# Performance work log

Hardware: AMD Instinct MI355X
Metric: run time of the kernel (lower is better)

The kernel has to match this reference:

```python
import jax, jax.numpy as jnp
import numpy as np

B, T, D_IN, D_EMB, H = 4, 2048, 1024, 1024, 16
HD = D_EMB // H  # head_dim = 64


def setup_inputs() -> dict:
    key = jax.random.key(0)
    k1, k2, k3 = jax.random.split(key, 3)
    scale_qkv = 1.0 / np.sqrt(D_IN)
    scale_o = 1.0 / np.sqrt(D_EMB)
    return {
        "x": jax.random.normal(k1, (B, T, D_IN), dtype=jnp.float32),
        "w_qkv": jax.random.normal(k2, (3 * D_EMB, D_IN), dtype=jnp.float32) * scale_qkv,
        "w_o": jax.random.normal(k3, (D_EMB, D_EMB), dtype=jnp.float32) * scale_o,
        "b_o": jnp.zeros((D_EMB,), dtype=jnp.float32),
    }


def reference(x, w_qkv, w_o, b_o):
    Bv, Tv, _ = x.shape
    # qkv projection: [B,T,3*D_EMB] -> [B,H,T,3*HD]
    qkv = jnp.einsum('btd,ed->bte', x, w_qkv)
    qkv = qkv.reshape(Bv, Tv, H, 3 * HD).transpose(0, 2, 1, 3)
    q, k, v = jnp.split(qkv, 3, axis=-1)  # each [B,H,T,HD]
    # scaled dot product with causal mask
    logits = jnp.einsum('bhqd,bhkd->bhqk', q, k) / np.sqrt(HD)
    causal = jnp.tril(jnp.ones((Tv, Tv), dtype=bool))
    logits = jnp.where(causal, logits, -jnp.inf)
    attn = jax.nn.softmax(logits, axis=-1)
    vals = jnp.einsum('bhqk,bhkd->bhqd', attn, v)
    vals = vals.transpose(0, 2, 1, 3).reshape(Bv, Tv, D_EMB)
    return jnp.einsum('bte,oe->bto', vals, w_o) + b_o
```

## Files before the change

### kernel.cpp

```cpp
#include <hip/hip_runtime.h>
#include <hip/hip_bf16.h>
#include <cstdint>
#include <cstddef>

#define B_    4
#define T_    2048
#define DIN_  1024
#define DEMB_ 1024
#define H_    16
#define HD_   64
#define M_    8192
#define NQKV_ 3072

#define QSCALE 0.18033688011112042f

typedef __bf16 bf16_t;
typedef __bf16 bf16x8 __attribute__((ext_vector_type(8)));
typedef __bf16 bf16x4 __attribute__((ext_vector_type(4)));
typedef float  f32x4  __attribute__((ext_vector_type(4)));
typedef float  f32x16 __attribute__((ext_vector_type(16)));
typedef unsigned int u32x4 __attribute__((ext_vector_type(4)));

__device__ __forceinline__ bf16_t tob(float f) {
  __hip_bfloat16 h = __float2bfloat16(f);
  return __builtin_bit_cast(bf16_t, h);
}

__device__ __forceinline__ f32x4 mfma16(bf16x8 a, bf16x8 b, f32x4 c) {
  return __builtin_amdgcn_mfma_f32_16x16x32_bf16(a, b, c, 0, 0, 0);
}
__device__ __forceinline__ f32x16 mfma32(bf16x8 a, bf16x8 b, f32x16 c) {
  return __builtin_amdgcn_mfma_f32_32x32x16_bf16(a, b, c, 0, 0, 0);
}

__device__ __forceinline__ float fexp2(float x) {
#if __has_builtin(__builtin_amdgcn_exp2f)
  return __builtin_amdgcn_exp2f(x);
#else
  return exp2f(x);
#endif
}

__device__ __forceinline__ unsigned pk2(float lo, float hi) {
  unsigned r;
  asm("v_cvt_pk_bf16_f32 %0, %1, %2" : "=v"(r) : "v"(lo), "v"(hi));
  return r;
}

__device__ __forceinline__ void plswap(unsigned& a, unsigned& b) {
  asm("v_permlane32_swap_b32 %0, %1" : "+v"(a), "+v"(b));
}

__device__ __forceinline__ void gload16(const void* g, void* l) {
  __builtin_amdgcn_global_load_lds((const __attribute__((address_space(1))) void*)g,
                                   (__attribute__((address_space(3))) void*)l, 16, 0, 0);
}

__global__ __launch_bounds__(256) void cast3_kernel(const float* __restrict__ a, bf16_t* __restrict__ ao,
                                                    const float* __restrict__ b, bf16_t* __restrict__ bo,
                                                    const float* __restrict__ c, bf16_t* __restrict__ co) {
  constexpr int na4 = M_ * DIN_ / 4;
  constexpr int nb4 = NQKV_ * DIN_ / 4;
  const int i = blockIdx.x * 256 + threadIdx.x;
  const float* src; bf16_t* dst; int off;
  if (i < na4)            { src = a; dst = ao; off = i; }
  else if (i < na4 + nb4) { src = b; dst = bo; off = i - na4; }
  else                    { src = c; dst = co; off = i - na4 - nb4; }
  float4 v = ((const float4*)src)[off];
  bf16x4 o;
  o[0] = tob(v.x); o[1] = tob(v.y); o[2] = tob(v.z); o[3] = tob(v.w);
  ((bf16x4*)dst)[off] = o;
}

__global__ __launch_bounds__(256, 3) void gemm_qkv_kernel(const bf16_t* __restrict__ A,
                                                          const bf16_t* __restrict__ Bm,
                                                          bf16_t* __restrict__ qb,
                                                          bf16_t* __restrict__ kb,
                                                          bf16_t* __restrict__ vbT) {
  constexpr int K = DIN_;
  __shared__ __align__(16) bf16_t As[128 * 64];
  __shared__ __align__(16) bf16_t Bs[128 * 64];
  const int tid = threadIdx.x, w = tid >> 6, l = tid & 63;
  const int lh = l >> 4, lr = l & 15;
  const int m0 = blockIdx.y * 128, n0 = blockIdx.x * 128;
  const int ar0 = (w >> 1) * 64, bc0 = (w & 1) * 64;
  f32x4 acc[4][4] = {};
  for (int k0 = 0; k0 < K; k0 += 64) {
#pragma unroll
    for (int i = 0; i < 4; ++i) {
      const int jx = i * 256 + tid;
      const int row = jx >> 3, us = (jx & 7) ^ (row & 7);
      gload16(A  + (size_t)(m0 + row) * K + k0 + us * 8, (char*)As + (size_t)(i * 256 + w * 64) * 16);
      gload16(Bm + (size_t)(n0 + row) * K + k0 + us * 8, (char*)Bs + (size_t)(i * 256 + w * 64) * 16);
    }
    __syncthreads();
#pragma unroll
    for (int kk = 0; kk < 2; ++kk) {
      bf16x8 af[4], bfv[4];
#pragma unroll
      for (int mi = 0; mi < 4; ++mi) {
        const int r = ar0 + mi * 16 + lr;
        af[mi] = *(const bf16x8*)&As[r * 64 + (((kk * 4 + lh) ^ (r & 7)) * 8)];
      }
#pragma unroll
      for (int ni = 0; ni < 4; ++ni) {
        const int r = bc0 + ni * 16 + lr;
        bfv[ni] = *(const bf16x8*)&Bs[r * 64 + (((kk * 4 + lh) ^ (r & 7)) * 8)];
      }
      __builtin_amdgcn_s_setprio(1);
#pragma unroll
      for (int mi = 0; mi < 4; ++mi)
#pragma unroll
        for (int ni = 0; ni < 4; ++ni)
          acc[mi][ni] = mfma16(af[mi], bfv[ni], acc[mi][ni]);
      __builtin_amdgcn_s_setprio(0);
    }
    __syncthreads();
  }
#pragma unroll
  for (int mi = 0; mi < 4; ++mi) {
    const int gm0 = m0 + ar0 + mi * 16 + lh * 4;
    const int bb = gm0 >> 11, t0 = gm0 & (T_ - 1);
#pragma unroll
    for (int ni = 0; ni < 4; ++ni) {
      const int gn = n0 + bc0 + ni * 16 + lr;
      const int h = gn / 192, s = gn - h * 192;
      const size_t bhb = (size_t)bb * H_ + h;
      if (s < 64) {
#pragma unroll
        for (int r = 0; r < 4; ++r)
          qb[(bhb * T_ + t0 + r) * HD_ + s] = tob(acc[mi][ni][r] * QSCALE);
      } else if (s < 128) {
#pragma unroll
        for (int r = 0; r < 4; ++r)
          kb[(bhb * T_ + t0 + r) * HD_ + s - 64] = tob(acc[mi][ni][r]);
      } else {
        bf16x4 pv;
#pragma unroll
        for (int r = 0; r < 4; ++r) pv[r] = tob(acc[mi][ni][r]);
        *(bf16x4*)&vbT[(bhb * HD_ + (s - 128)) * T_ + t0] = pv;
      }
    }
  }
}

__global__ __launch_bounds__(256, 2) void attn2_kernel(const bf16_t* __restrict__ qg,
                                                       const bf16_t* __restrict__ kg,
                                                       const bf16_t* __restrict__ vtg,
                                                       bf16_t* __restrict__ ob) {
  __shared__ __align__(16) bf16_t Kl[2][64 * 72];
  __shared__ __align__(16) bf16_t Vl[2][64 * 72];
  const int id = blockIdx.x;
  const int x  = (id >> 3) & 7;
  const int bh = (id & 7) | ((id >> 6) << 3);
  const int tid = threadIdx.x, w = tid >> 6, l = tid & 63;
  const int q5 = l & 31, hi = l >> 5, hi8 = hi * 8;
  const int srow = tid >> 3, scol = (tid & 7) * 8;
  const bf16_t* Qg  = qg  + (size_t)bh * T_ * HD_;
  const bf16_t* Kg  = kg  + (size_t)bh * T_ * HD_;
  const bf16_t* Vtg = vtg + (size_t)bh * HD_ * T_;

  for (int ph = 0; ph < 2; ++ph) {
    const int qt = ph ? (15 - x) : x;
    const int qb = qt * 128 + w * 32;
    const int ktmax = 2 * qt + 2;
    const int myKt  = qb >> 6;
    const int thrD  = qb + q5 - myKt * 64 - 4 * hi;

    bf16x8 bq[4];
#pragma unroll
    for (int s = 0; s < 4; ++s)
      bq[s] = *(const bf16x8*)&Qg[(size_t)(qb + q5) * HD_ + s * 16 + hi8];

    f32x16 o0 = {}, o1 = {};
    float lrun = 0.f;

    {
      *(bf16x8*)&Kl[0][srow * 72 + scol]        = *(const bf16x8*)&Kg[(size_t)srow * HD_ + scol];
      *(bf16x8*)&Kl[0][(srow + 32) * 72 + scol] = *(const bf16x8*)&Kg[(size_t)(srow + 32) * HD_ + scol];
      *(bf16x8*)&Vl[0][srow * 72 + scol]        = *(const bf16x8*)&Vtg[(size_t)srow * T_ + scol];
      *(bf16x8*)&Vl[0][(srow + 32) * 72 + scol] = *(const bf16x8*)&Vtg[(size_t)(srow + 32) * T_ + scol];
    }
    __syncthreads();
    int cur = 0;

    for (int kt = 0; kt < ktmax; ++kt) {
      const bool more = (kt + 1 < ktmax);
      bf16x8 nk0, nk1, nv0, nv1;
      if (more) {
        nk0 = *(const bf16x8*)&Kg[(size_t)((kt + 1) * 64 + srow) * HD_ + scol];
        nk1 = *(const bf16x8*)&Kg[(size_t)((kt + 1) * 64 + srow + 32) * HD_ + scol];
        nv0 = *(const bf16x8*)&Vtg[(size_t)srow * T_ + (kt + 1) * 64 + scol];
        nv1 = *(const bf16x8*)&Vtg[(size_t)(srow + 32) * T_ + (kt + 1) * 64 + scol];
      }
      if (kt <= myKt) {
        f32x16 sA = {}, sB = {};
        __builtin_amdgcn_s_setprio(1);
#pragma unroll
        for (int s = 0; s < 4; ++s) {
          bf16x8 a0 = *(const bf16x8*)&Kl[cur][(q5)      * 72 + s * 16 + hi8];
          bf16x8 a1 = *(const bf16x8*)&Kl[cur][(q5 + 32) * 72 + s * 16 + hi8];
          sA = mfma32(a0, bq[s], sA);
          sB = mfma32(a1, bq[s], sB);
        }
        __builtin_amdgcn_s_setprio(0);
        if (kt == myKt) {
#pragma unroll
          for (int r = 0; r < 16; ++r) {
            const int kvc = (r & 3) + 8 * (r >> 2);
            sA[r] = (kvc      > thrD) ? -1e30f : sA[r];
            sB[r] = (kvc + 32 > thrD) ? -1e30f : sB[r];
          }
        }
        float l0 = 0.f, l1 = 0.f, l2 = 0.f, l3 = 0.f;
#pragma unroll
        for (int r = 0; r < 16; r += 4) {
          sA[r]     = fexp2(sA[r]);     sB[r]     = fexp2(sB[r]);
          sA[r + 1] = fexp2(sA[r + 1]); sB[r + 1] = fexp2(sB[r + 1]);
          sA[r + 2] = fexp2(sA[r + 2]); sB[r + 2] = fexp2(sB[r + 2]);
          sA[r + 3] = fexp2(sA[r + 3]); sB[r + 3] = fexp2(sB[r + 3]);
          l0 += sA[r]     + sB[r];
          l1 += sA[r + 1] + sB[r + 1];
          l2 += sA[r + 2] + sB[r + 2];
          l3 += sA[r + 3] + sB[r + 3];
        }
        lrun += (l0 + l1) + (l2 + l3);
#pragma unroll
        for (int t32 = 0; t32 < 2; ++t32) {
          const f32x16& p = t32 ? sB : sA;
#pragma unroll
          for (int s2 = 0; s2 < 2; ++s2) {
            unsigned a0 = pk2(p[8 * s2 + 0], p[8 * s2 + 1]);
            unsigned a1 = pk2(p[8 * s2 + 2], p[8 * s2 + 3]);
            unsigned b0 = pk2(p[8 * s2 + 4], p[8 * s2 + 5]);
            unsigned b1 = pk2(p[8 * s2 + 6], p[8 * s2 + 7]);
            plswap(a0, b0);
            plswap(a1, b1);
            u32x4 fw = {a0, a1, b0, b1};
            const bf16x8 pb = __builtin_bit_cast(bf16x8, fw);
            const int kvo = t32 * 32 + s2 * 16 + hi8;
            bf16x8 av0 = *(const bf16x8*)&Vl[cur][(q5)      * 72 + kvo];
            bf16x8 av1 = *(const bf16x8*)&Vl[cur][(q5 + 32) * 72 + kvo];
            __builtin_amdgcn_s_setprio(1);
            o0 = mfma32(av0, pb, o0);
            o1 = mfma32(av1, pb, o1);
            __builtin_amdgcn_s_setprio(0);
          }
        }
      }
      if (more) {
        *(bf16x8*)&Kl[cur ^ 1][srow * 72 + scol]        = nk0;
        *(bf16x8*)&Kl[cur ^ 1][(srow + 32) * 72 + scol] = nk1;
        *(bf16x8*)&Vl[cur ^ 1][srow * 72 + scol]        = nv0;
        *(bf16x8*)&Vl[cur ^ 1][(srow + 32) * 72 + scol] = nv1;
      }
      __syncthreads();
      cur ^= 1;
    }

    const float ltot = lrun + __shfl_xor(lrun, 32);
    const float inv = 1.f / ltot;
    const size_t rowb = ((size_t)(bh >> 4) * T_ + qb + q5) * DEMB_ + (bh & 15) * HD_;
#pragma unroll
    for (int g = 0; g < 4; ++g) {
      bf16x4 st0, st1;
#pragma unroll
      for (int j = 0; j < 4; ++j) {
        st0[j] = tob(o0[4 * g + j] * inv);
        st1[j] = tob(o1[4 * g + j] * inv);
      }
      *(bf16x4*)&ob[rowb + 8 * g + 4 * hi]      = st0;
      *(bf16x4*)&ob[rowb + 8 * g + 4 * hi + 32] = st1;
    }
  }
}

__global__ __launch_bounds__(256, 3) void gemm_out_kernel(const bf16_t* __restrict__ A,
                                                          const bf16_t* __restrict__ Bm,
                                                          const float* __restrict__ bo,
                                                          float* __restrict__ out) {
  constexpr int K = DEMB_;
  __shared__ __align__(16) bf16_t As[128 * 64];
  __shared__ __align__(16) bf16_t Bs[128 * 64];
  const int tid = threadIdx.x, w = tid >> 6, l = tid & 63;
  const int lh = l >> 4, lr = l & 15;
  const int m0 = blockIdx.y * 128, n0 = blockIdx.x * 128;
  const int ar0 = (w >> 1) * 64, bc0 = (w & 1) * 64;
  f32x4 acc[4][4] = {};
  for (int k0 = 0; k0 < K; k0 += 64) {
#pragma unroll
    for (int i = 0; i < 4; ++i) {
      const int jx = i * 256 + tid;
      const int row = jx >> 3, us = (jx & 7) ^ (row & 7);
      gload16(A  + (size_t)(m0 + row) * K + k0 + us * 8, (char*)As + (size_t)(i * 256 + w * 64) * 16);
      gload16(Bm + (size_t)(n0 + row) * K + k0 + us * 8, (char*)Bs + (size_t)(i * 256 + w * 64) * 16);
    }
    __syncthreads();
#pragma unroll
    for (int kk = 0; kk < 2; ++kk) {
      bf16x8 af[4], bfv[4];
#pragma unroll
      for (int mi = 0; mi < 4; ++mi) {
        const int r = ar0 + mi * 16 + lr;
        af[mi] = *(const bf16x8*)&As[r * 64 + (((kk * 4 + lh) ^ (r & 7)) * 8)];
      }
#pragma unroll
      for (int ni = 0; ni < 4; ++ni) {
        const int r = bc0 + ni * 16 + lr;
        bfv[ni] = *(const bf16x8*)&Bs[r * 64 + (((kk * 4 + lh) ^ (r & 7)) * 8)];
      }
      __builtin_amdgcn_s_setprio(1);
#pragma unroll
      for (int mi = 0; mi < 4; ++mi)
#pragma unroll
        for (int ni = 0; ni < 4; ++ni)
          acc[mi][ni] = mfma16(af[mi], bfv[ni], acc[mi][ni]);
      __builtin_amdgcn_s_setprio(0);
    }
    __syncthreads();
  }
#pragma unroll
  for (int mi = 0; mi < 4; ++mi) {
#pragma unroll
    for (int r = 0; r < 4; ++r) {
      const int gm = m0 + ar0 + mi * 16 + lh * 4 + r;
#pragma unroll
      for (int ni = 0; ni < 4; ++ni) {
        const int gn = n0 + bc0 + ni * 16 + lr;
        out[(size_t)gm * DEMB_ + gn] = acc[mi][ni][r] + bo[gn];
      }
    }
  }
}

extern "C" void kernel_launch(void* const* d_in, const int* in_sizes, int n_in,
                              void* d_out, int out_size, void* d_ws, size_t ws_size,
                              hipStream_t stream) {
  (void)in_sizes; (void)n_in; (void)out_size; (void)ws_size;
  const float* x     = (const float*)d_in[0];
  const float* w_qkv = (const float*)d_in[1];
  const float* w_o   = (const float*)d_in[2];
  const float* b_o   = (const float*)d_in[3];
  float* out = (float*)d_out;

  char* p = (char*)d_ws;
  bf16_t* xb    = (bf16_t*)p; p += (size_t)M_ * DIN_ * 2;
  bf16_t* wqkvb = (bf16_t*)p; p += (size_t)NQKV_ * DIN_ * 2;
  bf16_t* wob   = (bf16_t*)p; p += (size_t)DEMB_ * DEMB_ * 2;
  bf16_t* qbuf  = (bf16_t*)p; p += (size_t)B_ * H_ * T_ * HD_ * 2;
  bf16_t* kbuf  = (bf16_t*)p; p += (size_t)B_ * H_ * T_ * HD_ * 2;
  bf16_t* vbuf  = (bf16_t*)p; p += (size_t)B_ * H_ * T_ * HD_ * 2;
  bf16_t* attnb = xb;

  constexpr int CAST_BLOCKS = (M_ * DIN_ + NQKV_ * DIN_ + DEMB_ * DEMB_) / 1024;
  cast3_kernel<<<CAST_BLOCKS, 256, 0, stream>>>(x, xb, w_qkv, wqkvb, w_o, wob);
  gemm_qkv_kernel<<<dim3(NQKV_ / 128, M_ / 128), 256, 0, stream>>>(xb, wqkvb, qbuf, kbuf, vbuf);
  attn2_kernel<<<512, 256, 0, stream>>>(qbuf, kbuf, vbuf, attnb);
  gemm_out_kernel<<<dim3(DEMB_ / 128, M_ / 128), 256, 0, stream>>>(attnb, wob, b_o, out);
}
```

Baseline: 153.8 us.

## Replace LDS-staged attention with single-wave blocks reading K/V from global

The attention kernel moves from 256-thread blocks that cooperatively staged K and V tiles in double-buffered shared memory to 64-thread single-wave blocks. Each wave loads its K and V MFMA operands directly from global memory (through the caches), with no LDS and no barriers. Each block handles a 32-row query strip and pairs strips st and 63-st to balance causal work. This removes synchronisation and the per-wave idle iterations, but K/V reuse across waves now depends on L1/L2 hits, and there is no explicit prefetch to hide global latency.

```diff
diff --git a/kernel.cpp b/kernel.cpp
--- a/kernel.cpp
+++ b/kernel.cpp
@@ -144,123 +144,94 @@
   }
 }
 
-__global__ __launch_bounds__(256, 2) void attn2_kernel(const bf16_t* __restrict__ qg,
-                                                       const bf16_t* __restrict__ kg,
-                                                       const bf16_t* __restrict__ vtg,
-                                                       bf16_t* __restrict__ ob) {
-  __shared__ __align__(16) bf16_t Kl[2][64 * 72];
-  __shared__ __align__(16) bf16_t Vl[2][64 * 72];
+__global__ __launch_bounds__(64) void attn3_kernel(const bf16_t* __restrict__ qg,
+                                                   const bf16_t* __restrict__ kg,
+                                                   const bf16_t* __restrict__ vtg,
+                                                   bf16_t* __restrict__ ob) {
   const int id = blockIdx.x;
-  const int x  = (id >> 3) & 7;
-  const int bh = (id & 7) | ((id >> 6) << 3);
-  const int tid = threadIdx.x, w = tid >> 6, l = tid & 63;
+  const int pp = (id >> 3) & 31;
+  const int bh = (id & 7) | ((id >> 8) << 3);
+  const int l = threadIdx.x;
   const int q5 = l & 31, hi = l >> 5, hi8 = hi * 8;
-  const int srow = tid >> 3, scol = (tid & 7) * 8;
   const bf16_t* Qg  = qg  + (size_t)bh * T_ * HD_;
   const bf16_t* Kg  = kg  + (size_t)bh * T_ * HD_;
   const bf16_t* Vtg = vtg + (size_t)bh * HD_ * T_;
 
   for (int ph = 0; ph < 2; ++ph) {
-    const int qt = ph ? (15 - x) : x;
-    const int qb = qt * 128 + w * 32;
-    const int ktmax = 2 * qt + 2;
-    const int myKt  = qb >> 6;
-    const int thrD  = qb + q5 - myKt * 64 - 4 * hi;
+    const int st = ph ? (63 - pp) : pp;
+    const int ktmax = (st >> 1) + 1;
+    const int myKt  = st >> 1;
+    const int thrD  = st * 32 + q5 - myKt * 64 - 4 * hi;
 
     bf16x8 bq[4];
 #pragma unroll
     for (int s = 0; s < 4; ++s)
-      bq[s] = *(const bf16x8*)&Qg[(size_t)(qb + q5) * HD_ + s * 16 + hi8];
+      bq[s] = *(const bf16x8*)&Qg[(size_t)(st * 32 + q5) * HD_ + s * 16 + hi8];
 
     f32x16 o0 = {}, o1 = {};
     float lrun = 0.f;
 
-    {
-      *(bf16x8*)&Kl[0][srow * 72 + scol]        = *(const bf16x8*)&Kg[(size_t)srow * HD_ + scol];
-      *(bf16x8*)&Kl[0][(srow + 32) * 72 + scol] = *(const bf16x8*)&Kg[(size_t)(srow + 32) * HD_ + scol];
-      *(bf16x8*)&Vl[0][srow * 72 + scol]        = *(const bf16x8*)&Vtg[(size_t)srow * T_ + scol];
-      *(bf16x8*)&Vl[0][(srow + 32) * 72 + scol] = *(const bf16x8*)&Vtg[(size_t)(srow + 32) * T_ + scol];
-    }
-    __syncthreads();
-    int cur = 0;
-
     for (int kt = 0; kt < ktmax; ++kt) {
-      const bool more = (kt + 1 < ktmax);
-      bf16x8 nk0, nk1, nv0, nv1;
-      if (more) {
-        nk0 = *(const bf16x8*)&Kg[(size_t)((kt + 1) * 64 + srow) * HD_ + scol];
-        nk1 = *(const bf16x8*)&Kg[(size_t)((kt + 1) * 64 + srow + 32) * HD_ + scol];
-        nv0 = *(const bf16x8*)&Vtg[(size_t)srow * T_ + (kt + 1) * 64 + scol];
-        nv1 = *(const bf16x8*)&Vtg[(size_t)(srow + 32) * T_ + (kt + 1) * 64 + scol];
-      }
-      if (kt <= myKt) {
-        f32x16 sA = {}, sB = {};
-        __builtin_amdgcn_s_setprio(1);
-#pragma unroll
-        for (int s = 0; s < 4; ++s) {
-          bf16x8 a0 = *(const bf16x8*)&Kl[cur][(q5)      * 72 + s * 16 + hi8];
-          bf16x8 a1 = *(const bf16x8*)&Kl[cur][(q5 + 32) * 72 + s * 16 + hi8];
-          sA = mfma32(a0, bq[s], sA);
-          sB = mfma32(a1, bq[s], sB);
+      f32x16 sA = {}, sB = {};
+#pragma unroll
+      for (int s = 0; s < 4; ++s) {
+        bf16x8 a0 = *(const bf16x8*)&Kg[(size_t)(kt * 64 + q5)      * HD_ + s * 16 + hi8];
+        bf16x8 a1 = *(const bf16x8*)&Kg[(size_t)(kt * 64 + q5 + 32) * HD_ + s * 16 + hi8];
+        sA = mfma32(a0, bq[s], sA);
+        sB = mfma32(a1, bq[s], sB);
+      }
+      bf16x8 avA[4], avB[4];
+#pragma unroll
+      for (int t32 = 0; t32 < 2; ++t32)
+#pragma unroll
+        for (int s2 = 0; s2 < 2; ++s2) {
+          const int kvo = kt * 64 + t32 * 32 + s2 * 16 + hi8;
+          avA[t32 * 2 + s2] = *(const bf16x8*)&Vtg[(size_t)(q5)      * T_ + kvo];
+          avB[t32 * 2 + s2] = *(const bf16x8*)&Vtg[(size_t)(q5 + 32) * T_ + kvo];
         }
-        __builtin_amdgcn_s_setprio(0);
-        if (kt == myKt) {
-#pragma unroll
-          for (int r = 0; r < 16; ++r) {
-            const int kvc = (r & 3) + 8 * (r >> 2);
-            sA[r] = (kvc      > thrD) ? -1e30f : sA[r];
-            sB[r] = (kvc + 32 > thrD) ? -1e30f : sB[r];
-          }
+      if (kt == myKt) {
+#pragma unroll
+        for (int r = 0; r < 16; ++r) {
+          const int kvc = (r & 3) + 8 * (r >> 2);
+          sA[r] = (kvc      > thrD) ? -1e30f : sA[r];
+          sB[r] = (kvc + 32 > thrD) ? -1e30f : sB[r];
         }
-        float l0 = 0.f, l1 = 0.f, l2 = 0.f, l3 = 0.f;
-#pragma unroll
-        for (int r = 0; r < 16; r += 4) {
-          sA[r]     = fexp2(sA[r]);     sB[r]     = fexp2(sB[r]);
-          sA[r + 1] = fexp2(sA[r + 1]); sB[r + 1] = fexp2(sB[r + 1]);
-          sA[r + 2] = fexp2(sA[r + 2]); sB[r + 2] = fexp2(sB[r + 2]);
-          sA[r + 3] = fexp2(sA[r + 3]); sB[r + 3] = fexp2(sB[r + 3]);
-          l0 += sA[r]     + sB[r];
-          l1 += sA[r + 1] + sB[r + 1];
-          l2 += sA[r + 2] + sB[r + 2];
-          l3 += sA[r + 3] + sB[r + 3];
+      }
+      float l0 = 0.f, l1 = 0.f, l2 = 0.f, l3 = 0.f;
+#pragma unroll
+      for (int r = 0; r < 16; r += 4) {
+        sA[r]     = fexp2(sA[r]);     sB[r]     = fexp2(sB[r]);
+        sA[r + 1] = fexp2(sA[r + 1]); sB[r + 1] = fexp2(sB[r + 1]);
+        sA[r + 2] = fexp2(sA[r + 2]); sB[r + 2] = fexp2(sB[r + 2]);
+        sA[r + 3] = fexp2(sA[r + 3]); sB[r + 3] = fexp2(sB[r + 3]);
+        l0 += sA[r]     + sB[r];
+        l1 += sA[r + 1] + sB[r + 1];
+        l2 += sA[r + 2] + sB[r + 2];
+        l3 += sA[r + 3] + sB[r + 3];
+      }
+      lrun += (l0 + l1) + (l2 + l3);
+#pragma unroll
+      for (int t32 = 0; t32 < 2; ++t32) {
+        const f32x16& p = t32 ? sB : sA;
+#pragma unroll
+        for (int s2 = 0; s2 < 2; ++s2) {
+          unsigned a0 = pk2(p[8 * s2 + 0], p[8 * s2 + 1]);
+          unsigned a1 = pk2(p[8 * s2 + 2], p[8 * s2 + 3]);
+          unsigned b0 = pk2(p[8 * s2 + 4], p[8 * s2 + 5]);
+          unsigned b1 = pk2(p[8 * s2 + 6], p[8 * s2 + 7]);
+          plswap(a0, b0);
+          plswap(a1, b1);
+          u32x4 fw = {a0, a1, b0, b1};
+          const bf16x8 pb = __builtin_bit_cast(bf16x8, fw);
+          o0 = mfma32(avA[t32 * 2 + s2], pb, o0);
+          o1 = mfma32(avB[t32 * 2 + s2], pb, o1);
         }
-        lrun += (l0 + l1) + (l2 + l3);
-#pragma unroll
-        for (int t32 = 0; t32 < 2; ++t32) {
-          const f32x16& p = t32 ? sB : sA;
-#pragma unroll
-          for (int s2 = 0; s2 < 2; ++s2) {
-            unsigned a0 = pk2(p[8 * s2 + 0], p[8 * s2 + 1]);
-            unsigned a1 = pk2(p[8 * s2 + 2], p[8 * s2 + 3]);
-            unsigned b0 = pk2(p[8 * s2 + 4], p[8 * s2 + 5]);
-            unsigned b1 = pk2(p[8 * s2 + 6], p[8 * s2 + 7]);
-            plswap(a0, b0);
-            plswap(a1, b1);
-            u32x4 fw = {a0, a1, b0, b1};
-            const bf16x8 pb = __builtin_bit_cast(bf16x8, fw);
-            const int kvo = t32 * 32 + s2 * 16 + hi8;
-            bf16x8 av0 = *(const bf16x8*)&Vl[cur][(q5)      * 72 + kvo];
-            bf16x8 av1 = *(const bf16x8*)&Vl[cur][(q5 + 32) * 72 + kvo];
-            __builtin_amdgcn_s_setprio(1);
-            o0 = mfma32(av0, pb, o0);
-            o1 = mfma32(av1, pb, o1);
-            __builtin_amdgcn_s_setprio(0);
-          }
-        }
-      }
-      if (more) {
-        *(bf16x8*)&Kl[cur ^ 1][srow * 72 + scol]        = nk0;
-        *(bf16x8*)&Kl[cur ^ 1][(srow + 32) * 72 + scol] = nk1;
-        *(bf16x8*)&Vl[cur ^ 1][srow * 72 + scol]        = nv0;
-        *(bf16x8*)&Vl[cur ^ 1][(srow + 32) * 72 + scol] = nv1;
-      }
-      __syncthreads();
-      cur ^= 1;
+      }
     }
 
     const float ltot = lrun + __shfl_xor(lrun, 32);
     const float inv = 1.f / ltot;
-    const size_t rowb = ((size_t)(bh >> 4) * T_ + qb + q5) * DEMB_ + (bh & 15) * HD_;
+    const size_t rowb = ((size_t)(bh >> 4) * T_ + st * 32 + q5) * DEMB_ + (bh & 15) * HD_;
 #pragma unroll
     for (int g = 0; g < 4; ++g) {
       bf16x4 st0, st1;
@@ -355,6 +326,6 @@
   constexpr int CAST_BLOCKS = (M_ * DIN_ + NQKV_ * DIN_ + DEMB_ * DEMB_) / 1024;
   cast3_kernel<<<CAST_BLOCKS, 256, 0, stream>>>(x, xb, w_qkv, wqkvb, w_o, wob);
   gemm_qkv_kernel<<<dim3(NQKV_ / 128, M_ / 128), 256, 0, stream>>>(xb, wqkvb, qbuf, kbuf, vbuf);
-  attn2_kernel<<<512, 256, 0, stream>>>(qbuf, kbuf, vbuf, attnb);
+  attn3_kernel<<<2048, 64, 0, stream>>>(qbuf, kbuf, vbuf, attnb);
   gemm_out_kernel<<<dim3(DEMB_ / 128, M_ / 128), 256, 0, stream>>>(attnb, wob, b_o, out);
 }
```

New measurement: 228.7 us. 48.6% more time.
